# Optimization experiments

Measured on AMD Instinct MI355X. Metric: run time of the kernel, lower is better.

Reference implementation:

```python
import jax, jax.numpy as jnp
import numpy as np

EMBED = 512
HEADS = 64
DK = EMBED // HEADS  # == n_wires_attn == 8
NW_FFN = 8
FFN = 2048
EPS = 1e-5


def _layernorm(x, g, b):
    mu = jnp.mean(x, axis=-1, keepdims=True)
    var = jnp.var(x, axis=-1, keepdims=True)
    return (x - mu) * jax.lax.rsqrt(var + EPS) * g + b


def setup_inputs() -> dict:
    key = jax.random.key(0)
    ks = jax.random.split(key, 12)
    d = {
        "x": jax.random.normal(ks[0], (4, 1024, EMBED), dtype=jnp.float32),
        # attention quantum RX params (one per wire, shared across heads/tokens)
        "phi": jax.random.normal(ks[1], (DK,), dtype=jnp.float32) * 0.1,
        # combine_heads linear
        "Wc": jax.random.normal(ks[2], (EMBED, EMBED), dtype=jnp.float32) / np.sqrt(EMBED),
        "bc": jnp.zeros((EMBED,), dtype=jnp.float32),
        # FFN quantum RY params
        "theta": jax.random.normal(ks[3], (NW_FFN,), dtype=jnp.float32) * 0.1,
        "W1": jax.random.normal(ks[4], (NW_FFN, FFN), dtype=jnp.float32) / np.sqrt(NW_FFN),
        "b1": jnp.zeros((FFN,), dtype=jnp.float32),
        "W2": jax.random.normal(ks[5], (FFN, EMBED), dtype=jnp.float32) / np.sqrt(FFN),
        "b2": jnp.zeros((EMBED,), dtype=jnp.float32),
        "g1": jnp.ones((EMBED,), dtype=jnp.float32),
        "be1": jnp.zeros((EMBED,), dtype=jnp.float32),
        "g2": jnp.ones((EMBED,), dtype=jnp.float32),
        "be2": jnp.zeros((EMBED,), dtype=jnp.float32),
    }
    return d


def reference(x, phi, Wc, bc, theta, W1, b1, W2, b2, g1, be1, g2, be2):
    B, S, E = x.shape
    # --- quantum attention projections ---
    # Per head-row of DK features: RX(x_i) encoder then trainable RX(phi_i),
    xh = x.reshape(B, S, HEADS, DK)
    qkv = jnp.cos(xh + phi)                     # [B,S,H,DK]
    qkv = jnp.transpose(qkv, (0, 2, 1, 3))      # [B,H,S,DK]
    scores = jnp.einsum('bhqd,bhkd->bhqk', qkv, qkv) / jnp.sqrt(jnp.float32(DK))
    attn = jax.nn.softmax(scores, axis=-1)
    out = jnp.einsum('bhqk,bhkd->bhqd', attn, qkv)
    out = jnp.transpose(out, (0, 2, 1, 3)).reshape(B, S, E)
    attn_out = out @ Wc.T if False else out @ Wc + bc  # combine_heads linear
    x1 = _layernorm(x + attn_out, g1, be1)
    # --- quantum FFN: RX(x_i) then trainable RY(theta_i) -> <Z> = cos(x_i)*cos(theta_i)
    qout = jnp.cos(x1[..., :NW_FFN]) * jnp.cos(theta)   # [B,S,NW_FFN]
    h = jax.nn.relu(qout @ W1 + b1)
    ffn_out = h @ W2 + b2
    return _layernorm(x1 + ffn_out, g2, be2)
```

## Files before the change

kernel.cpp:

```cpp
#include <hip/hip_runtime.h>
#include <hip/hip_bf16.h>
#include <math.h>

#define B 4
#define S 1024
#define E 512
#define H 64
#define DK 8
#define FFN 2048
#define BS (B*S)

#define CSCALE 0.7141879f

#if __has_builtin(__builtin_amdgcn_exp2f)
#define EXP2F(x) __builtin_amdgcn_exp2f(x)
#else
#define EXP2F(x) exp2f(x)
#endif

typedef __attribute__((ext_vector_type(8))) short short8;
typedef __attribute__((ext_vector_type(4))) float float4a;

union U8 { short8 v; unsigned u[4]; };
union F4 { float4a v; float f[4]; };

__device__ __forceinline__ unsigned short f2bf(float f) {
    unsigned u = __builtin_bit_cast(unsigned, f);
    u = (u + 0x7fffu + ((u >> 16) & 1u)) >> 16;
    return (unsigned short)u;
}
__device__ __forceinline__ float bf2f(unsigned short h) {
    return __builtin_bit_cast(float, (unsigned)h << 16);
}
__device__ __forceinline__ unsigned packbf(float a, float b) {
    return __builtin_amdgcn_perm(__builtin_bit_cast(unsigned, a),
                                 __builtin_bit_cast(unsigned, b), 0x07060302u);
}
__device__ __forceinline__ unsigned packbf_rn(float a, float b) {
    return ((unsigned)f2bf(a) << 16) | f2bf(b);
}
__device__ __forceinline__ int pidx(int k) {
    return (k & ~31) | (((k >> 2) & 3) << 3) | (((k >> 4) & 1) << 2) | (k & 3);
}

__device__ __forceinline__ void glds16(const void* g, void* l) {
    __builtin_amdgcn_global_load_lds(
        (const __attribute__((address_space(1))) void*)g,
        (__attribute__((address_space(3))) void*)l, 16, 0, 0);
}

__global__ __launch_bounds__(512) void attn_conv_kernel(const float* __restrict__ x,
                                                        const float* __restrict__ phi,
                                                        const float* __restrict__ Wc,
                                                        const float* __restrict__ W2,
                                                        const float* __restrict__ W1,
                                                        const float* __restrict__ b1,
                                                        unsigned short* __restrict__ Afrag,
                                                        unsigned short* __restrict__ W2f,
                                                        unsigned short* __restrict__ Wcf,
                                                        unsigned short* __restrict__ W1f) {
    __shared__ unsigned short kv[(S + 16) * DK];
    __shared__ unsigned short vtp[9][S + 8];
    int bid = blockIdx.x;
    int tid = threadIdx.x;
    const short8 z8 = {0,0,0,0,0,0,0,0};

    if (bid < 336) {
        int idx = bid * 512 + tid;
        if (idx < 131072) {
            int lane = idx & 63, c = idx >> 6;
            int ntile = c >> 6, kb32 = c & 63;
            int g = lane >> 4, col = lane & 15;
            int n = ntile * 16 + col, kb = kb32 * 32;
            short8 o;
            #pragma unroll
            for (int j = 0; j < 8; j++) {
                int k = kb + 16 * (j >> 2) + 4 * g + (j & 3);
                o[j] = (short)f2bf(W2[(size_t)k * 512 + n]);
            }
            *(short8*)&W2f[(size_t)idx * 8] = o;
        } else if (idx < 163840) {
            int i2 = idx - 131072;
            int lane = i2 & 63, c = i2 >> 6;
            int ntile = c >> 4, kb32 = c & 15;
            int g = lane >> 4, col = lane & 15;
            int n = ntile * 16 + col, kb = kb32 * 32;
            short8 o;
            #pragma unroll
            for (int j = 0; j < 8; j++)
                o[j] = (short)f2bf(Wc[(size_t)(kb + g * 8 + j) * 512 + n]);
            *(short8*)&Wcf[(size_t)i2 * 8] = o;
        } else {
            int i3 = idx - 163840;
            if (i3 < 4096) {
                int f = i3 >> 1, gg = i3 & 1;
                short8 o = z8;
                if (gg == 0) {
                    #pragma unroll
                    for (int j = 0; j < 8; j++) o[j] = (short)f2bf(W1[j * FFN + f]);
                } else {
                    o[0] = (short)f2bf(b1[f]);
                }
                *(short8*)&W1f[(size_t)i3 * 8] = o;
            }
        }
        return;
    }

    int abid = bid - 336;
    int head = abid >> 2, qquad = abid & 3;
    int b = head >> 6, hh = head & 63;

    float ph[DK];
    #pragma unroll
    for (int d = 0; d < DK; d++) ph[d] = phi[d];

    {
        int r2 = tid * 2;
        unsigned short vb[8][2];
        #pragma unroll
        for (int j = 0; j < 2; j++) {
            const float* xp = x + ((size_t)(b * S + r2 + j)) * E + hh * DK;
            float4 u = *(const float4*)xp;
            float4 v = *(const float4*)(xp + 4);
            float c[8] = {__cosf(u.x+ph[0]), __cosf(u.y+ph[1]), __cosf(u.z+ph[2]), __cosf(u.w+ph[3]),
                          __cosf(v.x+ph[4]), __cosf(v.y+ph[5]), __cosf(v.z+ph[6]), __cosf(v.w+ph[7])};
            U8 kr;
            kr.u[0] = packbf_rn(c[1] * CSCALE, c[0] * CSCALE);
            kr.u[1] = packbf_rn(c[3] * CSCALE, c[2] * CSCALE);
            kr.u[2] = packbf_rn(c[5] * CSCALE, c[4] * CSCALE);
            kr.u[3] = packbf_rn(c[7] * CSCALE, c[6] * CSCALE);
            *(short8*)&kv[(r2 + j) * DK] = kr.v;
            #pragma unroll
            for (int d = 0; d < 8; d++) vb[d][j] = f2bf(c[d]);
        }
        int pr = pidx(r2);
        #pragma unroll
        for (int d = 0; d < 8; d++)
            *(unsigned*)&vtp[d][pr] = (unsigned)vb[d][0] | ((unsigned)vb[d][1] << 16);
        *(unsigned*)&vtp[8][pr] = 0x3F803F80u;
    }
    if (tid < 16) *(short8*)&kv[(S + tid) * DK] = z8;
    __syncthreads();

    int w = tid >> 6, lane = tid & 63, col = lane & 15, g = lane >> 4;
    bool g0 = (g == 0);
    int q0 = qquad * 256 + w * 32;
    const float4a zc = {0.f,0.f,0.f,0.f};

    short8 aq[2];
    #pragma unroll
    for (int t = 0; t < 2; t++)
        aq[t] = g0 ? *(const short8*)&kv[(q0 + t*16 + col) * DK] : z8;

    float4a acc[2];
    acc[0] = zc; acc[1] = zc;

    int vrow = col < 8 ? col : 8;
    const unsigned short* vbase = &vtp[vrow][0];

    int off0 = g0 ? col * DK : S * DK;
    int off1 = g0 ? (16 + col) * DK : S * DK;
    int stepo = g0 ? 32 * DK : 0;

    for (int kb = 0; kb < S; kb += 32) {
        short8 bk0 = *(const short8*)&kv[off0];
        short8 bk1 = *(const short8*)&kv[off1];
        off0 += stepo; off1 += stepo;
        short8 vf = *(const short8*)(vbase + kb + g * 8);
        #pragma unroll
        for (int t = 0; t < 2; t++) {
            float4a s0 = __builtin_amdgcn_mfma_f32_16x16x32_bf16(bk0, aq[t], zc, 0,0,0);
            float4a s1 = __builtin_amdgcn_mfma_f32_16x16x32_bf16(bk1, aq[t], zc, 0,0,0);
            F4 S0, S1; S0.v = s0; S1.v = s1;
            float e00 = EXP2F(S0.f[0]);
            float e01 = EXP2F(S0.f[1]);
            float e02 = EXP2F(S0.f[2]);
            float e03 = EXP2F(S0.f[3]);
            float e10 = EXP2F(S1.f[0]);
            float e11 = EXP2F(S1.f[1]);
            float e12 = EXP2F(S1.f[2]);
            float e13 = EXP2F(S1.f[3]);
            U8 pf;
            pf.u[0] = packbf(e01, e00);
            pf.u[1] = packbf(e03, e02);
            pf.u[2] = packbf(e11, e10);
            pf.u[3] = packbf(e13, e12);
            acc[t] = __builtin_amdgcn_mfma_f32_16x16x32_bf16(vf, pf.v, acc[t], 0,0,0);
        }
    }
    int lp8 = ((hh & 3) * 16 + col) * 8;
    #pragma unroll
    for (int t = 0; t < 2; t++) {
        F4 a; a.v = acc[t];
        float denom = __shfl(a.f[0], 32 + col);
        float inv = __builtin_amdgcn_rcpf(denom);
        if (g < 2) {
            int chunk = (hh >> 2) * 256 + (b * 64 + qquad * 16 + w * 2 + t);
            uint2 o;
            o.x = packbf_rn(a.f[1] * inv, a.f[0] * inv);
            o.y = packbf_rn(a.f[3] * inv, a.f[2] * inv);
            *(uint2*)&Afrag[(size_t)chunk * 512 + lp8 + g * 4] = o;
        }
    }
}

__global__ __launch_bounds__(512) void combine_ln1(const unsigned short* __restrict__ Afrag,
                                                   const unsigned short* __restrict__ Wcf,
                                                   const float* __restrict__ bc,
                                                   const float* __restrict__ x,
                                                   const float* __restrict__ g1,
                                                   const float* __restrict__ be1,
                                                   float* __restrict__ x1out,
                                                   unsigned short* __restrict__ qoutbf,
                                                   const float* __restrict__ theta) {
    __shared__ unsigned short As[16 * 64 * 8];
    __shared__ unsigned short Wcs[2][2048 * 8];
    __shared__ float xout[16][516];
    int tt = blockIdx.x;
    int tid = threadIdx.x;
    int w = tid >> 6, lane = tid & 63;
    int wbase = (tid & ~63) * 8;

    #pragma unroll
    for (int r = 0; r < 2; r++) {
        const unsigned short* gsrc =
            Afrag + ((size_t)((r * 8 + w) * 256 + tt) * 64 + lane) * 8;
        glds16(gsrc, &As[r * 4096 + wbase]);
    }
    #pragma unroll
    for (int r = 0; r < 4; r++) {
        int nt = r * 8 + w;
        glds16(Wcf + ((size_t)(nt * 16 + 0) * 64 + lane) * 8, &Wcs[0][nt * 512]);
    }
    #pragma unroll
    for (int r = 0; r < 4; r++) {
        int nt = r * 8 + w;
        glds16(Wcf + ((size_t)(nt * 16 + 1) * 64 + lane) * 8, &Wcs[1][nt * 512]);
    }
    asm volatile("s_waitcnt vmcnt(4)" ::: "memory");
    __builtin_amdgcn_s_barrier();

    int col = lane & 15, g = lane >> 4;
    const float4a zc = {0.f,0.f,0.f,0.f};
    float4a acc[4];
    #pragma unroll
    for (int nt = 0; nt < 4; nt++) acc[nt] = zc;

    for (int kb32 = 0; kb32 < 16; kb32++) {
        int cur = kb32 & 1;
        short8 af = *(const short8*)&As[(kb32 * 64 + lane) * 8];
        #pragma unroll
        for (int nt = 0; nt < 4; nt++) {
            short8 bf = *(const short8*)&Wcs[cur][((w * 4 + nt) * 64 + lane) * 8];
            acc[nt] = __builtin_amdgcn_mfma_f32_16x16x32_bf16(af, bf, acc[nt], 0, 0, 0);
        }
        if (kb32 < 15) {
            asm volatile("s_waitcnt lgkmcnt(0)" ::: "memory");
            __builtin_amdgcn_s_barrier();
            if (kb32 < 14) {
                #pragma unroll
                for (int r = 0; r < 4; r++) {
                    int nt = r * 8 + w;
                    glds16(Wcf + ((size_t)(nt * 16 + kb32 + 2) * 64 + lane) * 8,
                           &Wcs[cur][nt * 512]);
                }
                asm volatile("s_waitcnt vmcnt(4)" ::: "memory");
            } else {
                asm volatile("s_waitcnt vmcnt(0)" ::: "memory");
            }
            __builtin_amdgcn_s_barrier();
        }
    }
    #pragma unroll
    for (int nt = 0; nt < 4; nt++) {
        int n = w * 64 + nt * 16 + col;
        float bb = bc[n];
        #pragma unroll
        for (int r = 0; r < 4; r++)
            xout[g * 4 + r][n] = acc[nt][r] + bb;
    }
    __syncthreads();

    int hl = lane >> 5, l = lane & 31;
    int token = w * 2 + hl;
    int e0 = l * 16;
    size_t grow = ((size_t)tt * 16 + token) * 512;
    float v[16];
    float s = 0.f, sq = 0.f;
    #pragma unroll
    for (int u = 0; u < 4; u++) {
        float4 xv = *(const float4*)&x[grow + e0 + u * 4];
        float4 pv = *(const float4*)&xout[token][e0 + u * 4];
        float a0 = xv.x + pv.x, a1 = xv.y + pv.y, a2 = xv.z + pv.z, a3 = xv.w + pv.w;
        v[u*4] = a0; v[u*4+1] = a1; v[u*4+2] = a2; v[u*4+3] = a3;
        s += a0 + a1 + a2 + a3;
        sq += a0*a0 + a1*a1 + a2*a2 + a3*a3;
    }
    #pragma unroll
    for (int off = 1; off <= 16; off <<= 1) {
        s  += __shfl_xor(s, off);
        sq += __shfl_xor(sq, off);
    }
    float mu = s * (1.f / 512.f);
    float var = sq * (1.f / 512.f) - mu * mu;
    float rstd = rsqrtf(var + 1e-5f);
    float y[16];
    #pragma unroll
    for (int u = 0; u < 4; u++) {
        float4 gv = *(const float4*)&g1[e0 + u * 4];
        float4 bv = *(const float4*)&be1[e0 + u * 4];
        y[u*4]   = (v[u*4]   - mu) * rstd * gv.x + bv.x;
        y[u*4+1] = (v[u*4+1] - mu) * rstd * gv.y + bv.y;
        y[u*4+2] = (v[u*4+2] - mu) * rstd * gv.z + bv.z;
        y[u*4+3] = (v[u*4+3] - mu) * rstd * gv.w + bv.w;
        float4 o = make_float4(y[u*4], y[u*4+1], y[u*4+2], y[u*4+3]);
        *(float4*)&x1out[grow + e0 + u * 4] = o;
    }
    if (l == 0) {
        U8 q;
        q.u[0] = packbf_rn(__cosf(y[1]) * __cosf(theta[1]), __cosf(y[0]) * __cosf(theta[0]));
        q.u[1] = packbf_rn(__cosf(y[3]) * __cosf(theta[3]), __cosf(y[2]) * __cosf(theta[2]));
        q.u[2] = packbf_rn(__cosf(y[5]) * __cosf(theta[5]), __cosf(y[4]) * __cosf(theta[4]));
        q.u[3] = packbf_rn(__cosf(y[7]) * __cosf(theta[7]), __cosf(y[6]) * __cosf(theta[6]));
        *(short8*)&qoutbf[((size_t)tt * 16 + token) * 8] = q.v;
    }
}

__global__ __launch_bounds__(512) void ffn_mfma(const unsigned short* __restrict__ qbf,
                                                const unsigned short* __restrict__ W1fg,
                                                const unsigned short* __restrict__ W2f,
                                                const float* __restrict__ b2,
                                                unsigned short* __restrict__ Cbf) {
    __shared__ unsigned short w1x[FFN * 16];
    int tid = threadIdx.x;
    int wbase = (tid & ~63) * 8;
    #pragma unroll
    for (int r = 0; r < 8; r++)
        glds16(W1fg + (size_t)(r * 512 + tid) * 8, &w1x[r * 4096 + wbase]);
    asm volatile("s_waitcnt vmcnt(0)" ::: "memory");
    __syncthreads();

    int w = tid >> 6, lane = tid & 63, col = lane & 15, g = lane >> 4;
    int mw = blockIdx.x * 128 + w * 16;
    int ntile = blockIdx.y;
    const short8 z8 = {0,0,0,0,0,0,0,0};
    const short8 one8 = {(short)0x3F80,0,0,0,0,0,0,0};
    const float4a zc = {0.f,0.f,0.f,0.f};

    short8 qf = (g == 0) ? *(const short8*)&qbf[(size_t)(mw + col) * 8]
                         : (g == 1 ? one8 : z8);
    float4a acc = zc;
    const unsigned short* w2p = W2f + (size_t)(ntile * 64) * 512 + lane * 8;

    #pragma unroll 2
    for (int kb32 = 0; kb32 < 64; kb32++) {
        int kb = kb32 * 32;
        short8 w1f0 = (g < 2) ? *(const short8*)&w1x[(kb + col) * 16 + g * 8] : z8;
        short8 w1f1 = (g < 2) ? *(const short8*)&w1x[(kb + 16 + col) * 16 + g * 8] : z8;
        short8 af = *(const short8*)(w2p + (size_t)kb32 * 512);
        float4a h0 = __builtin_amdgcn_mfma_f32_16x16x32_bf16(w1f0, qf, zc, 0,0,0);
        float4a h1 = __builtin_amdgcn_mfma_f32_16x16x32_bf16(w1f1, qf, zc, 0,0,0);
        F4 H0, H1; H0.v = h0; H1.v = h1;
        float e00 = fmaxf(H0.f[0], 0.f);
        float e01 = fmaxf(H0.f[1], 0.f);
        float e02 = fmaxf(H0.f[2], 0.f);
        float e03 = fmaxf(H0.f[3], 0.f);
        float e10 = fmaxf(H1.f[0], 0.f);
        float e11 = fmaxf(H1.f[1], 0.f);
        float e12 = fmaxf(H1.f[2], 0.f);
        float e13 = fmaxf(H1.f[3], 0.f);
        U8 pf;
        pf.u[0] = packbf(e01, e00);
        pf.u[1] = packbf(e03, e02);
        pf.u[2] = packbf(e11, e10);
        pf.u[3] = packbf(e13, e12);
        acc = __builtin_amdgcn_mfma_f32_16x16x32_bf16(af, pf.v, acc, 0,0,0);
    }
    int n0 = ntile * 16;
    F4 a; a.v = acc;
    float4 bb = *(const float4*)&b2[n0 + 4 * g];
    uint2 o;
    o.x = packbf_rn(a.f[1] + bb.y, a.f[0] + bb.x);
    o.y = packbf_rn(a.f[3] + bb.w, a.f[2] + bb.z);
    *(uint2*)&Cbf[(size_t)(mw + col) * 512 + n0 + 4 * g] = o;
}

__global__ __launch_bounds__(256) void ln_kernel(const float* a,
                                                 const unsigned short* __restrict__ r,
                                                 const float* __restrict__ g,
                                                 const float* __restrict__ be,
                                                 float* out) {
    int t = blockIdx.x, tid = threadIdx.x;
    size_t base = (size_t)t * E;
    int e0 = tid * 2;
    float2 av = *(const float2*)&a[base + e0];
    unsigned rv = *(const unsigned*)&r[base + e0];
    float v0 = av.x + bf2f((unsigned short)(rv & 0xffff));
    float v1 = av.y + bf2f((unsigned short)(rv >> 16));
    float s  = v0 + v1;
    float sq = v0 * v0 + v1 * v1;
    #pragma unroll
    for (int off = 32; off > 0; off >>= 1) {
        s  += __shfl_down(s, off);
        sq += __shfl_down(sq, off);
    }
    __shared__ float ls[4], lq[4];
    int wave = tid >> 6, lane = tid & 63;
    if (lane == 0) { ls[wave] = s; lq[wave] = sq; }
    __syncthreads();
    if (tid == 0) {
        float SS = ls[0] + ls[1] + ls[2] + ls[3];
        float QQ = lq[0] + lq[1] + lq[2] + lq[3];
        float mu = SS * (1.f / E);
        float var = QQ * (1.f / E) - mu * mu;
        ls[0] = mu;
        lq[0] = rsqrtf(var + 1e-5f);
    }
    __syncthreads();
    float mu = ls[0], rstd = lq[0];
    float2 gv = *(const float2*)&g[e0];
    float2 bv = *(const float2*)&be[e0];
    float y0 = (v0 - mu) * rstd * gv.x + bv.x;
    float y1 = (v1 - mu) * rstd * gv.y + bv.y;
    *(float2*)&out[base + e0] = make_float2(y0, y1);
}

extern "C" void kernel_launch(void* const* d_in, const int* in_sizes, int n_in,
                              void* d_out, int out_size, void* d_ws, size_t ws_size,
                              hipStream_t stream) {
    const float* x     = (const float*)d_in[0];
    const float* phi   = (const float*)d_in[1];
    const float* Wc    = (const float*)d_in[2];
    const float* bc    = (const float*)d_in[3];
    const float* theta = (const float*)d_in[4];
    const float* W1    = (const float*)d_in[5];
    const float* b1    = (const float*)d_in[6];
    const float* W2    = (const float*)d_in[7];
    const float* b2    = (const float*)d_in[8];
    const float* g1    = (const float*)d_in[9];
    const float* be1   = (const float*)d_in[10];
    const float* g2    = (const float*)d_in[11];
    const float* be2   = (const float*)d_in[12];
    float* out = (float*)d_out;

    float* ws = (float*)d_ws;
    unsigned short* Afrag  = (unsigned short*)ws;
    unsigned short* W2f    = (unsigned short*)(ws + 1048576);
    unsigned short* Wcf    = (unsigned short*)(ws + 1572864);
    unsigned short* W1f    = (unsigned short*)(ws + 1703936);
    unsigned short* qoutbf = (unsigned short*)(ws + 1736704);

    attn_conv_kernel<<<1360, 512, 0, stream>>>(x, phi, Wc, W2, W1, b1,
                                               Afrag, W2f, Wcf, W1f);
    combine_ln1<<<256, 512, 0, stream>>>(Afrag, Wcf, bc, x, g1, be1,
                                         out, qoutbf, theta);
    ffn_mfma<<<dim3(32, 32), 512, 0, stream>>>(qoutbf, W1f, W2f, b2, Afrag);
    ln_kernel<<<BS, 256, 0, stream>>>(out, Afrag, g2, be2, out);
}
```

Measured before the change: 185.4 us.

## Register-tile FFN MFMA kernel across tokens and N-tiles; wave-per-row final LayerNorm

The FFN kernel now gives each wave a 32-token by 4-N-tile output block. Each recomputed hidden fragment (the W1 product plus relu) is reused across four W2 MFMAs, and each W2 fragment is reused across two token tiles. W2 loads are double-buffered in registers, and the grid shrinks to 256 blocks of 256 threads, each staging W1 into LDS. This cuts redundant first-layer recompute, W1 LDS staging and W2 global reads, but raises register pressure and leaves fewer blocks for occupancy. The final LayerNorm now uses one wave per row with 8 elements per lane and xor shuffles, removing the LDS reduction and block barriers.

```diff
diff --git a/kernel.cpp b/kernel.cpp
--- a/kernel.cpp
+++ b/kernel.cpp
@@ -327,7 +327,7 @@
     }
 }
 
-__global__ __launch_bounds__(512) void ffn_mfma(const unsigned short* __restrict__ qbf,
+__global__ __launch_bounds__(256) void ffn_mfma(const unsigned short* __restrict__ qbf,
                                                 const unsigned short* __restrict__ W1fg,
                                                 const unsigned short* __restrict__ W2f,
                                                 const float* __restrict__ b2,
@@ -336,94 +336,145 @@
     int tid = threadIdx.x;
     int wbase = (tid & ~63) * 8;
     #pragma unroll
-    for (int r = 0; r < 8; r++)
-        glds16(W1fg + (size_t)(r * 512 + tid) * 8, &w1x[r * 4096 + wbase]);
+    for (int r = 0; r < 16; r++)
+        glds16(W1fg + (size_t)(r * 256 + tid) * 8, &w1x[r * 2048 + wbase]);
     asm volatile("s_waitcnt vmcnt(0)" ::: "memory");
     __syncthreads();
 
     int w = tid >> 6, lane = tid & 63, col = lane & 15, g = lane >> 4;
-    int mw = blockIdx.x * 128 + w * 16;
-    int ntile = blockIdx.y;
+    int tb = blockIdx.x >> 2, nb = blockIdx.x & 3;
+    int tg = w >> 1, ngw = w & 1;
+    int mw = tb * 64 + tg * 32;
+    int ntile0 = nb * 8 + ngw * 4;
     const short8 z8 = {0,0,0,0,0,0,0,0};
     const short8 one8 = {(short)0x3F80,0,0,0,0,0,0,0};
     const float4a zc = {0.f,0.f,0.f,0.f};
 
-    short8 qf = (g == 0) ? *(const short8*)&qbf[(size_t)(mw + col) * 8]
+    short8 qf[2];
+    #pragma unroll
+    for (int t = 0; t < 2; t++)
+        qf[t] = (g == 0) ? *(const short8*)&qbf[(size_t)(mw + t * 16 + col) * 8]
                          : (g == 1 ? one8 : z8);
-    float4a acc = zc;
-    const unsigned short* w2p = W2f + (size_t)(ntile * 64) * 512 + lane * 8;
-
-    #pragma unroll 2
-    for (int kb32 = 0; kb32 < 64; kb32++) {
-        int kb = kb32 * 32;
-        short8 w1f0 = (g < 2) ? *(const short8*)&w1x[(kb + col) * 16 + g * 8] : z8;
-        short8 w1f1 = (g < 2) ? *(const short8*)&w1x[(kb + 16 + col) * 16 + g * 8] : z8;
-        short8 af = *(const short8*)(w2p + (size_t)kb32 * 512);
-        float4a h0 = __builtin_amdgcn_mfma_f32_16x16x32_bf16(w1f0, qf, zc, 0,0,0);
-        float4a h1 = __builtin_amdgcn_mfma_f32_16x16x32_bf16(w1f1, qf, zc, 0,0,0);
-        F4 H0, H1; H0.v = h0; H1.v = h1;
-        float e00 = fmaxf(H0.f[0], 0.f);
-        float e01 = fmaxf(H0.f[1], 0.f);
-        float e02 = fmaxf(H0.f[2], 0.f);
-        float e03 = fmaxf(H0.f[3], 0.f);
-        float e10 = fmaxf(H1.f[0], 0.f);
-        float e11 = fmaxf(H1.f[1], 0.f);
-        float e12 = fmaxf(H1.f[2], 0.f);
-        float e13 = fmaxf(H1.f[3], 0.f);
-        U8 pf;
-        pf.u[0] = packbf(e01, e00);
-        pf.u[1] = packbf(e03, e02);
-        pf.u[2] = packbf(e11, e10);
-        pf.u[3] = packbf(e13, e12);
-        acc = __builtin_amdgcn_mfma_f32_16x16x32_bf16(af, pf.v, acc, 0,0,0);
-    }
-    int n0 = ntile * 16;
-    F4 a; a.v = acc;
-    float4 bb = *(const float4*)&b2[n0 + 4 * g];
-    uint2 o;
-    o.x = packbf_rn(a.f[1] + bb.y, a.f[0] + bb.x);
-    o.y = packbf_rn(a.f[3] + bb.w, a.f[2] + bb.z);
-    *(uint2*)&Cbf[(size_t)(mw + col) * 512 + n0 + 4 * g] = o;
-}
-
-__global__ __launch_bounds__(256) void ln_kernel(const float* a,
+
+    float4a acc[2][4];
+    #pragma unroll
+    for (int t = 0; t < 2; t++)
+        #pragma unroll
+        for (int nt = 0; nt < 4; nt++) acc[t][nt] = zc;
+
+    const unsigned short* w2p = W2f + (size_t)ntile0 * 64 * 512 + lane * 8;
+
+    short8 afA[4], afB[4];
+    #pragma unroll
+    for (int nt = 0; nt < 4; nt++)
+        afA[nt] = *(const short8*)(w2p + nt * 32768);
+
+#define FFN_BODY(KB32, AF)                                                        \
+    {                                                                             \
+        int kb = (KB32) * 32;                                                     \
+        short8 w1f0 = (g < 2) ? *(const short8*)&w1x[(kb + col) * 16 + g * 8] : z8;      \
+        short8 w1f1 = (g < 2) ? *(const short8*)&w1x[(kb + 16 + col) * 16 + g * 8] : z8; \
+        _Pragma("unroll")                                                         \
+        for (int t = 0; t < 2; t++) {                                             \
+            float4a h0 = __builtin_amdgcn_mfma_f32_16x16x32_bf16(w1f0, qf[t], zc, 0,0,0); \
+            float4a h1 = __builtin_amdgcn_mfma_f32_16x16x32_bf16(w1f1, qf[t], zc, 0,0,0); \
+            F4 H0, H1; H0.v = h0; H1.v = h1;                                      \
+            float e00 = fmaxf(H0.f[0], 0.f);                                      \
+            float e01 = fmaxf(H0.f[1], 0.f);                                      \
+            float e02 = fmaxf(H0.f[2], 0.f);                                      \
+            float e03 = fmaxf(H0.f[3], 0.f);                                      \
+            float e10 = fmaxf(H1.f[0], 0.f);                                      \
+            float e11 = fmaxf(H1.f[1], 0.f);                                      \
+            float e12 = fmaxf(H1.f[2], 0.f);                                      \
+            float e13 = fmaxf(H1.f[3], 0.f);                                      \
+            U8 pf;                                                                \
+            pf.u[0] = packbf(e01, e00);                                           \
+            pf.u[1] = packbf(e03, e02);                                           \
+            pf.u[2] = packbf(e11, e10);                                           \
+            pf.u[3] = packbf(e13, e12);                                           \
+            _Pragma("unroll")                                                     \
+            for (int nt = 0; nt < 4; nt++)                                        \
+                acc[t][nt] = __builtin_amdgcn_mfma_f32_16x16x32_bf16(AF[nt], pf.v, \
+                                                                     acc[t][nt], 0,0,0); \
+        }                                                                         \
+    }
+
+    for (int kb32 = 0; kb32 < 64; kb32 += 2) {
+        #pragma unroll
+        for (int nt = 0; nt < 4; nt++)
+            afB[nt] = *(const short8*)(w2p + nt * 32768 + (kb32 + 1) * 512);
+        FFN_BODY(kb32, afA)
+        if (kb32 + 2 < 64) {
+            #pragma unroll
+            for (int nt = 0; nt < 4; nt++)
+                afA[nt] = *(const short8*)(w2p + nt * 32768 + (kb32 + 2) * 512);
+        }
+        FFN_BODY(kb32 + 1, afB)
+    }
+#undef FFN_BODY
+
+    int n0 = ntile0 * 16;
+    #pragma unroll
+    for (int nt = 0; nt < 4; nt++) {
+        float4 bb = *(const float4*)&b2[n0 + nt * 16 + 4 * g];
+        #pragma unroll
+        for (int t = 0; t < 2; t++) {
+            F4 a; a.v = acc[t][nt];
+            uint2 o;
+            o.x = packbf_rn(a.f[1] + bb.y, a.f[0] + bb.x);
+            o.y = packbf_rn(a.f[3] + bb.w, a.f[2] + bb.z);
+            *(uint2*)&Cbf[(size_t)(mw + t * 16 + col) * 512 + n0 + nt * 16 + 4 * g] = o;
+        }
+    }
+}
+
+__global__ __launch_bounds__(256) void ln_kernel(const float* __restrict__ a,
                                                  const unsigned short* __restrict__ r,
                                                  const float* __restrict__ g,
                                                  const float* __restrict__ be,
-                                                 float* out) {
-    int t = blockIdx.x, tid = threadIdx.x;
+                                                 float* __restrict__ out) {
+    int t = blockIdx.x * 4 + (threadIdx.x >> 6);
+    int lane = threadIdx.x & 63;
     size_t base = (size_t)t * E;
-    int e0 = tid * 2;
-    float2 av = *(const float2*)&a[base + e0];
-    unsigned rv = *(const unsigned*)&r[base + e0];
-    float v0 = av.x + bf2f((unsigned short)(rv & 0xffff));
-    float v1 = av.y + bf2f((unsigned short)(rv >> 16));
-    float s  = v0 + v1;
-    float sq = v0 * v0 + v1 * v1;
-    #pragma unroll
-    for (int off = 32; off > 0; off >>= 1) {
-        s  += __shfl_down(s, off);
-        sq += __shfl_down(sq, off);
-    }
-    __shared__ float ls[4], lq[4];
-    int wave = tid >> 6, lane = tid & 63;
-    if (lane == 0) { ls[wave] = s; lq[wave] = sq; }
-    __syncthreads();
-    if (tid == 0) {
-        float SS = ls[0] + ls[1] + ls[2] + ls[3];
-        float QQ = lq[0] + lq[1] + lq[2] + lq[3];
-        float mu = SS * (1.f / E);
-        float var = QQ * (1.f / E) - mu * mu;
-        ls[0] = mu;
-        lq[0] = rsqrtf(var + 1e-5f);
-    }
-    __syncthreads();
-    float mu = ls[0], rstd = lq[0];
-    float2 gv = *(const float2*)&g[e0];
-    float2 bv = *(const float2*)&be[e0];
-    float y0 = (v0 - mu) * rstd * gv.x + bv.x;
-    float y1 = (v1 - mu) * rstd * gv.y + bv.y;
-    *(float2*)&out[base + e0] = make_float2(y0, y1);
+    int e0 = lane * 8;
+    float4 a0 = *(const float4*)&a[base + e0];
+    float4 a1 = *(const float4*)&a[base + e0 + 4];
+    uint4 rv = *(const uint4*)&r[base + e0];
+    float v[8];
+    v[0] = a0.x + bf2f((unsigned short)(rv.x & 0xffff));
+    v[1] = a0.y + bf2f((unsigned short)(rv.x >> 16));
+    v[2] = a0.z + bf2f((unsigned short)(rv.y & 0xffff));
+    v[3] = a0.w + bf2f((unsigned short)(rv.y >> 16));
+    v[4] = a1.x + bf2f((unsigned short)(rv.z & 0xffff));
+    v[5] = a1.y + bf2f((unsigned short)(rv.z >> 16));
+    v[6] = a1.z + bf2f((unsigned short)(rv.w & 0xffff));
+    v[7] = a1.w + bf2f((unsigned short)(rv.w >> 16));
+    float s = 0.f, sq = 0.f;
+    #pragma unroll
+    for (int i = 0; i < 8; i++) { s += v[i]; sq += v[i] * v[i]; }
+    #pragma unroll
+    for (int off = 1; off <= 32; off <<= 1) {
+        s  += __shfl_xor(s, off);
+        sq += __shfl_xor(sq, off);
+    }
+    float mu = s * (1.f / E);
+    float var = sq * (1.f / E) - mu * mu;
+    float rstd = rsqrtf(var + 1e-5f);
+    float4 g0 = *(const float4*)&g[e0];
+    float4 g1v = *(const float4*)&g[e0 + 4];
+    float4 b0 = *(const float4*)&be[e0];
+    float4 b1v = *(const float4*)&be[e0 + 4];
+    float4 o0, o1;
+    o0.x = (v[0] - mu) * rstd * g0.x + b0.x;
+    o0.y = (v[1] - mu) * rstd * g0.y + b0.y;
+    o0.z = (v[2] - mu) * rstd * g0.z + b0.z;
+    o0.w = (v[3] - mu) * rstd * g0.w + b0.w;
+    o1.x = (v[4] - mu) * rstd * g1v.x + b1v.x;
+    o1.y = (v[5] - mu) * rstd * g1v.y + b1v.y;
+    o1.z = (v[6] - mu) * rstd * g1v.z + b1v.z;
+    o1.w = (v[7] - mu) * rstd * g1v.w + b1v.w;
+    *(float4*)&out[base + e0] = o0;
+    *(float4*)&out[base + e0 + 4] = o1;
 }
 
 extern "C" void kernel_launch(void* const* d_in, const int* in_sizes, int n_in,
@@ -455,6 +506,6 @@
                                                Afrag, W2f, Wcf, W1f);
     combine_ln1<<<256, 512, 0, stream>>>(Afrag, Wcf, bc, x, g1, be1,
                                          out, qoutbf, theta);
-    ffn_mfma<<<dim3(32, 32), 512, 0, stream>>>(qoutbf, W1f, W2f, b2, Afrag);
-    ln_kernel<<<BS, 256, 0, stream>>>(out, Afrag, g2, be2, out);
-}
+    ffn_mfma<<<256, 256, 0, stream>>>(qoutbf, W1f, W2f, b2, Afrag);
+    ln_kernel<<<1024, 256, 0, stream>>>(out, Afrag, g2, be2, out);
+}
```

Result: faster. 164.1 us (-11.5%).
